# Kernel optimization log

Hardware: AMD Instinct MI355X
Metric: run time of the kernel (lower is better)

The kernel has to match this reference:

```python
import jax, jax.numpy as jnp
import numpy as np

D_MODEL = 1024
N_HEAD = 16
D_HEAD = D_MODEL // N_HEAD


def setup_inputs() -> dict:
    key = jax.random.key(0)
    ks = jax.random.split(key, 5)
    x = jax.random.normal(ks[0], (4, 2048, D_MODEL), dtype=jnp.float32)
    # qkv linear: weight [3*d_model, d_model], bias [3*d_model] (torch convention)
    w_qkv = jax.random.normal(ks[1], (3 * D_MODEL, D_MODEL), dtype=jnp.float32) / np.sqrt(D_MODEL)
    b_qkv = jnp.zeros((3 * D_MODEL,), dtype=jnp.float32)
    w_proj = jax.random.normal(ks[2], (D_MODEL, D_MODEL), dtype=jnp.float32) / np.sqrt(D_MODEL)
    b_proj = jnp.zeros((D_MODEL,), dtype=jnp.float32)
    return {"x": x, "w_qkv": w_qkv, "b_qkv": b_qkv, "w_proj": w_proj, "b_proj": b_proj}


def reference(x, w_qkv, b_qkv, w_proj, b_proj):
    B, T, C = x.shape
    qkv = x @ w_qkv.T + b_qkv  # [B,T,3C]
    q, k, v = jnp.split(qkv, 3, axis=-1)
    # [B, H, T, Dh]
    q = q.reshape(B, T, N_HEAD, D_HEAD).transpose(0, 2, 1, 3)
    k = k.reshape(B, T, N_HEAD, D_HEAD).transpose(0, 2, 1, 3)
    v = v.reshape(B, T, N_HEAD, D_HEAD).transpose(0, 2, 1, 3)
    att = jnp.einsum('bhqd,bhkd->bhqk', q, k) / jnp.sqrt(jnp.float32(D_HEAD))
    causal = jnp.tril(jnp.ones((T, T), dtype=bool))  # [T,T]
    att = jnp.where(causal, att, -jnp.inf)
    att = jax.nn.softmax(att, axis=-1)
    y = jnp.einsum('bhqk,bhkd->bhqd', att, v)  # [B,H,T,Dh]
    y = y.transpose(0, 2, 1, 3).reshape(B, T, C)
    return y @ w_proj.T + b_proj
```

## Files before the change

kernel.cpp:

```cpp
#include <hip/hip_runtime.h>
#include <hip/hip_bf16.h>

#define DEV static __device__ __forceinline__

typedef __attribute__((ext_vector_type(8))) short short8;
typedef __attribute__((ext_vector_type(4))) short short4v;
typedef __attribute__((ext_vector_type(4))) float float4v;
typedef __attribute__((ext_vector_type(4))) int int4v;

DEV unsigned short f2bf(float f) {
  unsigned int u = __builtin_bit_cast(unsigned int, f);
  u = (u + 0x7fffu + ((u >> 16) & 1u)) >> 16;
  return (unsigned short)u;
}

DEV __attribute__((address_space(3))) void* to_lds(void* p) {
  return (__attribute__((address_space(3))) void*)p;
}
DEV const __attribute__((address_space(1))) void* to_glb(const void* p) {
  return (const __attribute__((address_space(1))) void*)p;
}

DEV float4v zero4() { float4v z = {0.f, 0.f, 0.f, 0.f}; return z; }

DEV float ex2(float x) {
  float r;
  asm("v_exp_f32 %0, %1" : "=v"(r) : "v"(x));
  return r;
}
DEV unsigned int cvtpk(float lo, float hi) {
  unsigned int r;
  asm("v_cvt_pk_bf16_f32 %0, %1, %2" : "=v"(r) : "v"(lo), "v"(hi));
  return r;
}

__global__ __launch_bounds__(256)
void f32_to_bf16_kn(const float* __restrict__ src, unsigned short* __restrict__ dst, int n) {
  int i = (blockIdx.x * blockDim.x + threadIdx.x) * 4;
  int stride = gridDim.x * blockDim.x * 4;
  for (; i < n; i += stride) {
    float4v v = *reinterpret_cast<const float4v*>(src + i);
    short4v o;
    o[0] = (short)f2bf(v[0]);
    o[1] = (short)f2bf(v[1]);
    o[2] = (short)f2bf(v[2]);
    o[3] = (short)f2bf(v[3]);
    *reinterpret_cast<short4v*>(dst + i) = o;
  }
}

template<int EPI>
__global__ __launch_bounds__(256, 2)
void gemm_bt_kn(const unsigned short* __restrict__ A, const unsigned short* __restrict__ B,
                const float* __restrict__ bias, void* __restrict__ Cout,
                unsigned short* __restrict__ vtout, int M, int N, int K) {
  __shared__ unsigned short sA[128 * 64];
  __shared__ unsigned short sB[128 * 64];
  const int t = threadIdx.x;
  const int wave = t >> 6, lane = t & 63;
  const int wm = wave >> 1, wn = wave & 1;
  const int nwg = gridDim.x * gridDim.y;
  const int lid = blockIdx.y * gridDim.x + blockIdx.x;
  const int swz = (lid & 7) * (nwg >> 3) + (lid >> 3);
  const int m0 = (swz / gridDim.x) * 128, n0 = (swz % gridDim.x) * 128;
  const int l15 = lane & 15, l4 = lane >> 4;

  float4v acc[4][4];
#pragma unroll
  for (int i = 0; i < 4; i++)
#pragma unroll
    for (int j = 0; j < 4; j++) acc[i][j] = zero4();

  const int row_s = t >> 3;
  const int cols_s = ((t & 7) ^ ((t >> 3) & 7)) * 8;

  for (int k0 = 0; k0 < K; k0 += 64) {
    __syncthreads();
#pragma unroll
    for (int i = 0; i < 4; i++) {
      const unsigned short* ga = &A[(size_t)(m0 + row_s + i * 32) * K + k0 + cols_s];
      __builtin_amdgcn_global_load_lds(to_glb(ga), to_lds(&sA[(i * 4096 + wave * 1024) / 2]), 16, 0, 0);
    }
#pragma unroll
    for (int i = 0; i < 4; i++) {
      const unsigned short* gb = &B[(size_t)(n0 + row_s + i * 32) * K + k0 + cols_s];
      __builtin_amdgcn_global_load_lds(to_glb(gb), to_lds(&sB[(i * 4096 + wave * 1024) / 2]), 16, 0, 0);
    }
    __syncthreads();
#pragma unroll
    for (int kc = 0; kc < 2; kc++) {
      short8 af[4], bf[4];
#pragma unroll
      for (int mf = 0; mf < 4; mf++) {
        int off = ((wm * 64 + mf * 16 + l15) * 128 + kc * 64 + l4 * 16) ^ ((l15 & 7) << 4);
        af[mf] = *reinterpret_cast<const short8*>((const char*)sA + off);
      }
#pragma unroll
      for (int nf = 0; nf < 4; nf++) {
        int off = ((wn * 64 + nf * 16 + l15) * 128 + kc * 64 + l4 * 16) ^ ((l15 & 7) << 4);
        bf[nf] = *reinterpret_cast<const short8*>((const char*)sB + off);
      }
      __builtin_amdgcn_s_setprio(1);
#pragma unroll
      for (int mf = 0; mf < 4; mf++)
#pragma unroll
        for (int nf = 0; nf < 4; nf++)
          acc[mf][nf] = __builtin_amdgcn_mfma_f32_16x16x32_bf16(af[mf], bf[nf], acc[mf][nf], 0, 0, 0);
      __builtin_amdgcn_s_setprio(0);
    }
  }

#pragma unroll
  for (int mf = 0; mf < 4; mf++) {
    const int row0 = m0 + wm * 64 + mf * 16 + l4 * 4;
#pragma unroll
    for (int nf = 0; nf < 4; nf++) {
      const int col = n0 + wn * 64 + nf * 16 + l15;
      float vv[4];
#pragma unroll
      for (int r = 0; r < 4; r++) vv[r] = acc[mf][nf][r] + bias[col];
      if (EPI == 1) {
#pragma unroll
        for (int r = 0; r < 4; r++)
          ((float*)Cout)[(size_t)(row0 + r) * N + col] = vv[r];
      } else {
        if (col < 2048) {
          const float s = (col < 1024) ? 0.18033688f : 1.0f;
#pragma unroll
          for (int r = 0; r < 4; r++)
            ((unsigned short*)Cout)[(size_t)(row0 + r) * 2048 + col] = f2bf(vv[r] * s);
        } else {
          const int hv = col - 2048;
          const int R = ((row0 >> 11) * 16 + (hv >> 6)) * 64 + (hv & 63);
          const int tc = row0 & 2047;
          unsigned long long w = (unsigned long long)cvtpk(vv[0], vv[1]) |
                                 ((unsigned long long)cvtpk(vv[2], vv[3]) << 32);
          *(unsigned long long*)&vtout[(size_t)R * 2048 + tc] = w;
        }
      }
    }
  }
}

__global__ __launch_bounds__(256, 3)
void attn_kn(const unsigned short* __restrict__ qk, const unsigned short* __restrict__ vt,
             unsigned short* __restrict__ y) {
  __shared__ unsigned short sK[2][4096];
  __shared__ unsigned short sV[2][4096];
  __shared__ unsigned short sP[4][2048];
  const int t = threadIdx.x;
  const int wave = t >> 6, lane = t & 63;
  const int l15 = lane & 15, l4 = lane >> 4;
  const int bh = blockIdx.x, b = bh >> 4, h = bh & 15;
  const int yb_ = blockIdx.y;
  const int qt = ((yb_ >> 2) & 1) ? ((yb_ < 8) ? yb_ + 4 : yb_ - 12) : 15 - yb_;
  const int q0w = qt * 128 + wave * 32;
  const size_t base = (size_t)b * 2048 * 2048;
  const unsigned short* Qp = qk + base + h * 64;
  const unsigned short* Kp = Qp + 1024;
  const unsigned short* Vt = vt + (size_t)bh * 64 * 2048;
  unsigned short* yb = y + (size_t)b * 2048 * 1024 + h * 64;

  short8 ones8;
#pragma unroll
  for (int j = 0; j < 8; j++) ones8[j] = (short)0x3F80;

  short8 qf[2][2];
#pragma unroll
  for (int m = 0; m < 2; m++)
#pragma unroll
    for (int kc = 0; kc < 2; kc++)
      qf[m][kc] = *reinterpret_cast<const short8*>(
          &Qp[(size_t)(q0w + m * 16 + l15) * 2048 + kc * 32 + l4 * 8]);

  float4v o_acc[2][4];
#pragma unroll
  for (int m = 0; m < 2; m++)
#pragma unroll
    for (int f = 0; f < 4; f++) o_acc[m][f] = zero4();
  float4v acc_l[2] = {zero4(), zero4()};

  auto stage_k = [&](int kv0, int bi) {
#pragma unroll
    for (int i = 0; i < 2; i++) {
      int unit = t + i * 256;
      int row = unit >> 3, sl = unit & 7;
      const unsigned short* g = Kp + (size_t)(kv0 + row) * 2048 + (sl ^ (row & 7)) * 8;
      __builtin_amdgcn_global_load_lds(to_glb(g), to_lds(&sK[bi][unit * 8]), 16, 0, 0);
    }
  };
  auto stage_v = [&](int kv0, int bi) {
#pragma unroll
    for (int i = 0; i < 2; i++) {
      int unit = t + i * 256;
      int d = unit >> 3, sl = unit & 7;
      const unsigned short* g = Vt + (size_t)d * 2048 + kv0 + (sl ^ (d & 7)) * 8;
      __builtin_amdgcn_global_load_lds(to_glb(g), to_lds(&sV[bi][unit * 8]), 16, 0, 0);
    }
  };

  const int nt = 2 * qt + 2;
  stage_k(0, 0);
  stage_v(0, 0);
  __syncthreads();

  for (int ti = 0; ti < nt; ti++) {
    const int cur = ti & 1;
    const int kv0 = ti * 64;
    const bool last = (ti + 1 == nt);
    if (!last) { stage_k(kv0 + 64, cur ^ 1); stage_v(kv0 + 64, cur ^ 1); }

    if (kv0 <= q0w + 31) {
      const char* Kb = (const char*)sK[cur];
      const char* Vb = (const char*)sV[cur];
      char* Pb = (char*)sP[wave];

      float4v st[2][4];
#pragma unroll
      for (int m = 0; m < 2; m++)
#pragma unroll
        for (int c = 0; c < 4; c++) st[m][c] = zero4();
#pragma unroll
      for (int kc = 0; kc < 2; kc++) {
        short8 ka[4];
#pragma unroll
        for (int c = 0; c < 4; c++) {
          int off = ((c * 16 + l15) * 128 + kc * 64 + l4 * 16) ^ ((l15 & 7) << 4);
          ka[c] = *reinterpret_cast<const short8*>(Kb + off);
        }
        __builtin_amdgcn_s_setprio(1);
#pragma unroll
        for (int c = 0; c < 4; c++) {
          st[0][c] = __builtin_amdgcn_mfma_f32_16x16x32_bf16(ka[c], qf[0][kc], st[0][c], 0, 0, 0);
          st[1][c] = __builtin_amdgcn_mfma_f32_16x16x32_bf16(ka[c], qf[1][kc], st[1][c], 0, 0, 0);
        }
        __builtin_amdgcn_s_setprio(0);
      }

#pragma unroll
      for (int m = 0; m < 2; m++) {
        if (kv0 + 63 > q0w + m * 16) {
          const int qrow = q0w + m * 16 + l15;
#pragma unroll
          for (int c = 0; c < 4; c++)
#pragma unroll
            for (int r = 0; r < 4; r++) {
              int kv = kv0 + c * 16 + l4 * 4 + r;
              if (kv > qrow) st[m][c][r] = -1e30f;
            }
        }
#pragma unroll
        for (int c = 0; c < 4; c++) {
          float p0 = ex2(st[m][c][0]), p1 = ex2(st[m][c][1]);
          float p2 = ex2(st[m][c][2]), p3 = ex2(st[m][c][3]);
          unsigned long long w = (unsigned long long)cvtpk(p0, p1) |
                                 ((unsigned long long)cvtpk(p2, p3) << 32);
          int off = ((m * 16 + l15) * 128 + (c * 16 + l4 * 4) * 2) ^ ((l15 & 7) << 4);
          *(unsigned long long*)(Pb + off) = w;
        }
      }
      asm volatile("s_waitcnt lgkmcnt(0)" ::: "memory");
      __builtin_amdgcn_sched_barrier(0);

#pragma unroll
      for (int kc = 0; kc < 2; kc++) {
        short8 pa[2];
#pragma unroll
        for (int m = 0; m < 2; m++) {
          int off = ((m * 16 + l15) * 128 + kc * 64 + l4 * 16) ^ ((l15 & 7) << 4);
          pa[m] = *reinterpret_cast<const short8*>(Pb + off);
        }
        short8 vbf[4];
#pragma unroll
        for (int f = 0; f < 4; f++) {
          int d = f * 16 + l15;
          int off = (d * 128 + kc * 64 + l4 * 16) ^ ((d & 7) << 4);
          vbf[f] = *reinterpret_cast<const short8*>(Vb + off);
        }
        __builtin_amdgcn_s_setprio(1);
#pragma unroll
        for (int f = 0; f < 4; f++) {
          o_acc[0][f] = __builtin_amdgcn_mfma_f32_16x16x32_bf16(pa[0], vbf[f], o_acc[0][f], 0, 0, 0);
          o_acc[1][f] = __builtin_amdgcn_mfma_f32_16x16x32_bf16(pa[1], vbf[f], o_acc[1][f], 0, 0, 0);
        }
        acc_l[0] = __builtin_amdgcn_mfma_f32_16x16x32_bf16(pa[0], ones8, acc_l[0], 0, 0, 0);
        acc_l[1] = __builtin_amdgcn_mfma_f32_16x16x32_bf16(pa[1], ones8, acc_l[1], 0, 0, 0);
        __builtin_amdgcn_s_setprio(0);
      }
    }
    __syncthreads();
  }

#pragma unroll
  for (int m = 0; m < 2; m++) {
    float lr[4];
#pragma unroll
    for (int r = 0; r < 4; r++) lr[r] = 1.0f / acc_l[m][r];
#pragma unroll
    for (int f = 0; f < 4; f++)
#pragma unroll
      for (int r = 0; r < 4; r++) {
        int q = q0w + m * 16 + l4 * 4 + r;
        yb[(size_t)q * 1024 + f * 16 + l15] = f2bf(o_acc[m][f][r] * lr[r]);
      }
  }
}

extern "C" void kernel_launch(void* const* d_in, const int* in_sizes, int n_in,
                              void* d_out, int out_size, void* d_ws, size_t ws_size,
                              hipStream_t stream) {
  const float* x = (const float*)d_in[0];
  const float* w_qkv = (const float*)d_in[1];
  const float* b_qkv = (const float*)d_in[2];
  const float* w_proj = (const float*)d_in[3];
  const float* b_proj = (const float*)d_in[4];
  float* out = (float*)d_out;
  char* ws = (char*)d_ws;

  const int M = 4 * 2048;
  unsigned short* x_bf = (unsigned short*)ws;
  unsigned short* wqkv_bf = (unsigned short*)(ws + (22ull << 20));
  unsigned short* wproj_bf = (unsigned short*)(ws + (28ull << 20));
  unsigned short* qk_buf = (unsigned short*)(ws + (30ull << 20));
  unsigned short* vt = (unsigned short*)(ws + (62ull << 20));
  unsigned short* y_bf = x_bf;

  f32_to_bf16_kn<<<2048, 256, 0, stream>>>(x, x_bf, M * 1024);
  f32_to_bf16_kn<<<1024, 256, 0, stream>>>(w_qkv, wqkv_bf, 3072 * 1024);
  f32_to_bf16_kn<<<512, 256, 0, stream>>>(w_proj, wproj_bf, 1024 * 1024);

  gemm_bt_kn<2><<<dim3(3072 / 128, M / 128), 256, 0, stream>>>(
      x_bf, wqkv_bf, b_qkv, qk_buf, vt, M, 3072, 1024);

  attn_kn<<<dim3(64, 16), 256, 0, stream>>>(qk_buf, vt, y_bf);

  gemm_bt_kn<1><<<dim3(1024 / 128, M / 128), 256, 0, stream>>>(
      y_bf, wproj_bf, b_proj, out, nullptr, M, 1024, 1024);
}
```

Before: 157.0 us.

## Use 256-row double-buffered GEMM tiles with prefetch for QKV and projection

Result: no change. 157.7 us (+0.5%).

```diff
diff --git a/kernel.cpp b/kernel.cpp
--- a/kernel.cpp
+++ b/kernel.cpp
@@ -49,73 +49,110 @@
   }
 }
 
-template<int EPI>
-__global__ __launch_bounds__(256, 2)
-void gemm_bt_kn(const unsigned short* __restrict__ A, const unsigned short* __restrict__ B,
-                const float* __restrict__ bias, void* __restrict__ Cout,
-                unsigned short* __restrict__ vtout, int M, int N, int K) {
-  __shared__ unsigned short sA[128 * 64];
-  __shared__ unsigned short sB[128 * 64];
+template<int BN, int WM, int WN, int EPI>
+DEV void gemm256_body(const unsigned short* __restrict__ A, const unsigned short* __restrict__ B,
+                      const float* __restrict__ bias, void* __restrict__ Cout,
+                      unsigned short* __restrict__ vtout, int M, int N, int K,
+                      unsigned short* sAraw, unsigned short* sBraw) {
+  constexpr int MF = 256 / (WM * 16);
+  constexpr int NF = BN / (WN * 16);
+  constexpr int BPASS = BN / 64;
   const int t = threadIdx.x;
-  const int wave = t >> 6, lane = t & 63;
-  const int wm = wave >> 1, wn = wave & 1;
-  const int nwg = gridDim.x * gridDim.y;
-  const int lid = blockIdx.y * gridDim.x + blockIdx.x;
+  const int lane = t & 63;
+  const int wid = t >> 6;
+  const int l15 = lane & 15, l4 = lane >> 4;
+  const int wm = wid / WN, wn = wid % WN;
+  const int wrow = wm * MF * 16, wcol = wn * NF * 16;
+  const int gx = gridDim.x;
+  const int nwg = gx * gridDim.y;
+  const int lid = blockIdx.y * gx + blockIdx.x;
   const int swz = (lid & 7) * (nwg >> 3) + (lid >> 3);
-  const int m0 = (swz / gridDim.x) * 128, n0 = (swz % gridDim.x) * 128;
-  const int l15 = lane & 15, l4 = lane >> 4;
-
-  float4v acc[4][4];
-#pragma unroll
-  for (int i = 0; i < 4; i++)
-#pragma unroll
-    for (int j = 0; j < 4; j++) acc[i][j] = zero4();
-
-  const int row_s = t >> 3;
-  const int cols_s = ((t & 7) ^ ((t >> 3) & 7)) * 8;
-
-  for (int k0 = 0; k0 < K; k0 += 64) {
-    __syncthreads();
+  const int m0 = (swz / gx) * 256, n0 = (swz % gx) * BN;
+  const int lkey = (l15 & 7) << 4;
+
+  float4v acc[MF][NF];
+#pragma unroll
+  for (int i = 0; i < MF; i++)
+#pragma unroll
+    for (int j = 0; j < NF; j++) acc[i][j] = zero4();
+
+  auto stage = [&](int bi, int k0) {
 #pragma unroll
     for (int i = 0; i < 4; i++) {
-      const unsigned short* ga = &A[(size_t)(m0 + row_s + i * 32) * K + k0 + cols_s];
-      __builtin_amdgcn_global_load_lds(to_glb(ga), to_lds(&sA[(i * 4096 + wave * 1024) / 2]), 16, 0, 0);
-    }
-#pragma unroll
-    for (int i = 0; i < 4; i++) {
-      const unsigned short* gb = &B[(size_t)(n0 + row_s + i * 32) * K + k0 + cols_s];
-      __builtin_amdgcn_global_load_lds(to_glb(gb), to_lds(&sB[(i * 4096 + wave * 1024) / 2]), 16, 0, 0);
-    }
-    __syncthreads();
-#pragma unroll
-    for (int kc = 0; kc < 2; kc++) {
-      short8 af[4], bf[4];
-#pragma unroll
-      for (int mf = 0; mf < 4; mf++) {
-        int off = ((wm * 64 + mf * 16 + l15) * 128 + kc * 64 + l4 * 16) ^ ((l15 & 7) << 4);
-        af[mf] = *reinterpret_cast<const short8*>((const char*)sA + off);
-      }
-#pragma unroll
-      for (int nf = 0; nf < 4; nf++) {
-        int off = ((wn * 64 + nf * 16 + l15) * 128 + kc * 64 + l4 * 16) ^ ((l15 & 7) << 4);
-        bf[nf] = *reinterpret_cast<const short8*>((const char*)sB + off);
-      }
+      int unit = t + i * 512;
+      int row = unit >> 3, sl = unit & 7;
+      const unsigned short* g = &A[(size_t)(m0 + row) * K + k0 + (sl ^ (row & 7)) * 8];
+      __builtin_amdgcn_global_load_lds(to_glb(g), to_lds(&sAraw[bi * 256 * 64 + unit * 8]), 16, 0, 0);
+    }
+#pragma unroll
+    for (int i = 0; i < BPASS; i++) {
+      int unit = t + i * 512;
+      int row = unit >> 3, sl = unit & 7;
+      const unsigned short* g = &B[(size_t)(n0 + row) * K + k0 + (sl ^ (row & 7)) * 8];
+      __builtin_amdgcn_global_load_lds(to_glb(g), to_lds(&sBraw[bi * BN * 64 + unit * 8]), 16, 0, 0);
+    }
+  };
+
+  stage(0, 0);
+  const int nk = K >> 6;
+  for (int s = 0; s < nk; ++s) {
+    const int cur = s & 1;
+    if (s + 1 < nk) {
+      stage(cur ^ 1, (s + 1) << 6);
+      if constexpr (BPASS == 3)
+        asm volatile("s_waitcnt vmcnt(7)");
+      else
+        asm volatile("s_waitcnt vmcnt(6)");
+    } else {
+      asm volatile("s_waitcnt vmcnt(0)");
+    }
+    __builtin_amdgcn_sched_barrier(0);
+    __builtin_amdgcn_s_barrier();
+    __builtin_amdgcn_sched_barrier(0);
+
+    const char* Ab = (const char*)&sAraw[cur * 256 * 64];
+    const char* Bb = (const char*)&sBraw[cur * BN * 64];
+    short8 bfr[NF][2];
+#pragma unroll
+    for (int nf = 0; nf < NF; nf++)
+#pragma unroll
+      for (int kc = 0; kc < 2; kc++) {
+        int off = ((wcol + nf * 16 + l15) * 128 + kc * 64 + l4 * 16) ^ lkey;
+        bfr[nf][kc] = *reinterpret_cast<const short8*>(Bb + off);
+      }
+#pragma unroll
+    for (int g = 0; g < MF; g += 4) {
+      short8 afr[4][2];
+#pragma unroll
+      for (int i = 0; i < 4; i++)
+#pragma unroll
+        for (int kc = 0; kc < 2; kc++) {
+          int off = ((wrow + (g + i) * 16 + l15) * 128 + kc * 64 + l4 * 16) ^ lkey;
+          afr[i][kc] = *reinterpret_cast<const short8*>(Ab + off);
+        }
       __builtin_amdgcn_s_setprio(1);
 #pragma unroll
-      for (int mf = 0; mf < 4; mf++)
-#pragma unroll
-        for (int nf = 0; nf < 4; nf++)
-          acc[mf][nf] = __builtin_amdgcn_mfma_f32_16x16x32_bf16(af[mf], bf[nf], acc[mf][nf], 0, 0, 0);
+      for (int kc = 0; kc < 2; kc++)
+#pragma unroll
+        for (int i = 0; i < 4; i++)
+#pragma unroll
+          for (int nf = 0; nf < NF; nf++)
+            acc[g + i][nf] =
+                __builtin_amdgcn_mfma_f32_16x16x32_bf16(afr[i][kc], bfr[nf][kc], acc[g + i][nf], 0, 0, 0);
       __builtin_amdgcn_s_setprio(0);
     }
-  }
-
-#pragma unroll
-  for (int mf = 0; mf < 4; mf++) {
-    const int row0 = m0 + wm * 64 + mf * 16 + l4 * 4;
-#pragma unroll
-    for (int nf = 0; nf < 4; nf++) {
-      const int col = n0 + wn * 64 + nf * 16 + l15;
+    asm volatile("s_waitcnt lgkmcnt(0)" ::: "memory");
+    __builtin_amdgcn_sched_barrier(0);
+    __builtin_amdgcn_s_barrier();
+    __builtin_amdgcn_sched_barrier(0);
+  }
+
+#pragma unroll
+  for (int mf = 0; mf < MF; mf++) {
+    const int row0 = m0 + wrow + mf * 16 + l4 * 4;
+#pragma unroll
+    for (int nf = 0; nf < NF; nf++) {
+      const int col = n0 + wcol + nf * 16 + l15;
       float vv[4];
 #pragma unroll
       for (int r = 0; r < 4; r++) vv[r] = acc[mf][nf][r] + bias[col];
@@ -125,10 +162,10 @@
           ((float*)Cout)[(size_t)(row0 + r) * N + col] = vv[r];
       } else {
         if (col < 2048) {
-          const float s = (col < 1024) ? 0.18033688f : 1.0f;
+          const float sc = (col < 1024) ? 0.18033688f : 1.0f;
 #pragma unroll
           for (int r = 0; r < 4; r++)
-            ((unsigned short*)Cout)[(size_t)(row0 + r) * 2048 + col] = f2bf(vv[r] * s);
+            ((unsigned short*)Cout)[(size_t)(row0 + r) * 2048 + col] = f2bf(vv[r] * sc);
         } else {
           const int hv = col - 2048;
           const int R = ((row0 >> 11) * 16 + (hv >> 6)) * 64 + (hv & 63);
@@ -140,6 +177,24 @@
       }
     }
   }
+}
+
+__global__ __launch_bounds__(512, 2)
+void gemm256_qkv_kn(const unsigned short* __restrict__ A, const unsigned short* __restrict__ B,
+                    const float* __restrict__ bias, unsigned short* __restrict__ qkout,
+                    unsigned short* __restrict__ vtout, int M, int N, int K) {
+  __shared__ unsigned short sA[2][256 * 64];
+  __shared__ unsigned short sB[2][192 * 64];
+  gemm256_body<192, 2, 4, 2>(A, B, bias, qkout, vtout, M, N, K, &sA[0][0], &sB[0][0]);
+}
+
+__global__ __launch_bounds__(512, 2)
+void gemm256_proj_kn(const unsigned short* __restrict__ A, const unsigned short* __restrict__ B,
+                     const float* __restrict__ bias, float* __restrict__ Cout,
+                     int M, int N, int K) {
+  __shared__ unsigned short sA[2][256 * 64];
+  __shared__ unsigned short sB[2][128 * 64];
+  gemm256_body<128, 4, 2, 1>(A, B, bias, Cout, nullptr, M, N, K, &sA[0][0], &sB[0][0]);
 }
 
 __global__ __launch_bounds__(256, 3)
@@ -329,11 +384,11 @@
   f32_to_bf16_kn<<<1024, 256, 0, stream>>>(w_qkv, wqkv_bf, 3072 * 1024);
   f32_to_bf16_kn<<<512, 256, 0, stream>>>(w_proj, wproj_bf, 1024 * 1024);
 
-  gemm_bt_kn<2><<<dim3(3072 / 128, M / 128), 256, 0, stream>>>(
+  gemm256_qkv_kn<<<dim3(16, 32), 512, 0, stream>>>(
       x_bf, wqkv_bf, b_qkv, qk_buf, vt, M, 3072, 1024);
 
   attn_kn<<<dim3(64, 16), 256, 0, stream>>>(qk_buf, vt, y_bf);
 
-  gemm_bt_kn<1><<<dim3(1024 / 128, M / 128), 256, 0, stream>>>(
-      y_bf, wproj_bf, b_proj, out, nullptr, M, 1024, 1024);
-}
+  gemm256_proj_kn<<<dim3(8, 32), 512, 0, stream>>>(
+      y_bf, wproj_bf, b_proj, out, M, 1024, 1024);
+}
```

## Replace GEMMs with 8-wave double-buffered 256-row tile kernels with interleaved loads

Applied to the files above, without the earlier changes.

Result: no change. 160.0 us (+1.9%).

```diff
diff --git a/kernel.cpp b/kernel.cpp
--- a/kernel.cpp
+++ b/kernel.cpp
@@ -49,73 +49,145 @@
   }
 }
 
-template<int EPI>
-__global__ __launch_bounds__(256, 2)
-void gemm_bt_kn(const unsigned short* __restrict__ A, const unsigned short* __restrict__ B,
-                const float* __restrict__ bias, void* __restrict__ Cout,
-                unsigned short* __restrict__ vtout, int M, int N, int K) {
-  __shared__ unsigned short sA[128 * 64];
-  __shared__ unsigned short sB[128 * 64];
-  const int t = threadIdx.x;
-  const int wave = t >> 6, lane = t & 63;
-  const int wm = wave >> 1, wn = wave & 1;
-  const int nwg = gridDim.x * gridDim.y;
-  const int lid = blockIdx.y * gridDim.x + blockIdx.x;
+template<int NF, int EPI>
+DEV void gemm8p_body(const unsigned short* __restrict__ A, const unsigned short* __restrict__ B,
+                     const float* __restrict__ bias, void* __restrict__ Cout,
+                     unsigned short* __restrict__ vtout, int M, int N, int K,
+                     unsigned short* sA, unsigned short* sB) {
+  constexpr int BN = NF * 64;
+  const int t = threadIdx.x, lane = t & 63, wid = t >> 6;
+  const int l15 = lane & 15, l4 = lane >> 4;
+  const int wm = wid >> 2, wn = wid & 3;
+  const int wrow = wm * 128, wcol = wn * NF * 16;
+  const int gx = gridDim.x, nwg = gx * gridDim.y;
+  const int lid = blockIdx.y * gx + blockIdx.x;
   const int swz = (lid & 7) * (nwg >> 3) + (lid >> 3);
-  const int m0 = (swz / gridDim.x) * 128, n0 = (swz % gridDim.x) * 128;
-  const int l15 = lane & 15, l4 = lane >> 4;
-
-  float4v acc[4][4];
-#pragma unroll
-  for (int i = 0; i < 4; i++)
-#pragma unroll
-    for (int j = 0; j < 4; j++) acc[i][j] = zero4();
-
-  const int row_s = t >> 3;
-  const int cols_s = ((t & 7) ^ ((t >> 3) & 7)) * 8;
-
-  for (int k0 = 0; k0 < K; k0 += 64) {
-    __syncthreads();
-#pragma unroll
-    for (int i = 0; i < 4; i++) {
-      const unsigned short* ga = &A[(size_t)(m0 + row_s + i * 32) * K + k0 + cols_s];
-      __builtin_amdgcn_global_load_lds(to_glb(ga), to_lds(&sA[(i * 4096 + wave * 1024) / 2]), 16, 0, 0);
+  const int m0 = (swz / gx) * 256, n0 = (swz % gx) * BN;
+  const int lkey = (l15 & 7) << 4;
+
+  float4v acc[8][NF];
+#pragma unroll
+  for (int i = 0; i < 8; i++)
+#pragma unroll
+    for (int j = 0; j < NF; j++) acc[i][j] = zero4();
+
+  auto stB = [&](int buf, int k0, int pass) {
+    int u = t + pass * 512, row = u >> 3, sl = u & 7;
+    const unsigned short* g = &B[(size_t)(n0 + row) * K + k0 + (sl ^ (row & 7)) * 8];
+    __builtin_amdgcn_global_load_lds(to_glb(g), to_lds(&sB[buf * BN * 64 + u * 8]), 16, 0, 0);
+  };
+  auto stA = [&](int buf, int k0, int q) {
+    int r6 = t >> 3, sl = t & 7;
+    int row = 32 * q + (r6 & 31) + 128 * (r6 >> 5);
+    const unsigned short* g = &A[(size_t)(m0 + row) * K + k0 + (sl ^ (row & 7)) * 8];
+    __builtin_amdgcn_global_load_lds(to_glb(g), to_lds(&sA[buf * 256 * 64 + row * 64 + sl * 8]), 16, 0, 0);
+  };
+  short8 af[2][2], bfr[NF][2];
+  auto rdA = [&](const char* Ab, int q) {
+#pragma unroll
+    for (int fi = 0; fi < 2; fi++)
+#pragma unroll
+      for (int kc = 0; kc < 2; kc++) {
+        int off = ((wrow + (q * 2 + fi) * 16 + l15) * 128 + kc * 64 + l4 * 16) ^ lkey;
+        af[fi][kc] = *reinterpret_cast<const short8*>(Ab + off);
+      }
+  };
+  auto rdB = [&](const char* Bb) {
+#pragma unroll
+    for (int nf = 0; nf < NF; nf++)
+#pragma unroll
+      for (int kc = 0; kc < 2; kc++) {
+        int off = ((wcol + nf * 16 + l15) * 128 + kc * 64 + l4 * 16) ^ lkey;
+        bfr[nf][kc] = *reinterpret_cast<const short8*>(Bb + off);
+      }
+  };
+
+#define MMQ(Q)                                                                           \
+  do {                                                                                   \
+    __builtin_amdgcn_s_setprio(1);                                                       \
+    _Pragma("unroll") for (int kc = 0; kc < 2; kc++)                                     \
+        _Pragma("unroll") for (int fi = 0; fi < 2; fi++)                                 \
+            _Pragma("unroll") for (int nf = 0; nf < NF; nf++) acc[(Q)*2 + fi][nf] =      \
+        __builtin_amdgcn_mfma_f32_16x16x32_bf16(af[fi][kc], bfr[nf][kc],                 \
+                                                acc[(Q)*2 + fi][nf], 0, 0, 0);           \
+    __builtin_amdgcn_s_setprio(0);                                                       \
+  } while (0)
+#define BARR __builtin_amdgcn_s_barrier()
+#define LGKM0 asm volatile("s_waitcnt lgkmcnt(0)" ::: "memory")
+#define VMW(N) asm volatile("s_waitcnt vmcnt(" #N ")" ::: "memory")
+
+#pragma unroll
+  for (int p = 0; p < NF; p++) stB(0, 0, p);
+#pragma unroll
+  for (int q = 0; q < 4; q++) stA(0, 0, q);
+  VMW(3);
+  BARR;
+
+  const char* Ab0 = (const char*)&sA[0];
+  const char* Bb0 = (const char*)&sB[0];
+  const char* Ab1 = (const char*)&sA[256 * 64];
+  const char* Bb1 = (const char*)&sB[BN * 64];
+  const int NI = K >> 7;
+
+  for (int i = 0; i < NI; ++i) {
+    const int k1 = (i << 7) + 64, k2 = (i << 7) + 128;
+    const bool nl = (i + 1 < NI);
+    rdB(Bb0);
+    rdA(Ab0, 0);
+    stB(1, k1, 0);
+    stB(1, k1, 1);
+    VMW(4);
+    BARR; LGKM0; MMQ(0); BARR;
+    rdA(Ab0, 1);
+    if (NF == 3) { stB(1, k1, 2); stA(1, k1, 0); }
+    else { stA(1, k1, 0); stA(1, k1, 1); }
+    VMW(5);
+    BARR; LGKM0; MMQ(1); BARR;
+    rdA(Ab0, 2);
+    if (NF == 3) { stA(1, k1, 1); stA(1, k1, 2); }
+    else { stA(1, k1, 2); stA(1, k1, 3); }
+    VMW(6);
+    BARR; LGKM0; MMQ(2); BARR;
+    rdA(Ab0, 3);
+    if (NF == 3) stA(1, k1, 3);
+    VMW(3);
+    BARR; LGKM0; MMQ(3); BARR;
+    rdB(Bb1);
+    rdA(Ab1, 0);
+    if (nl) { stB(0, k2, 0); stB(0, k2, 1); VMW(4); } else { VMW(2); }
+    BARR; LGKM0; MMQ(0); BARR;
+    rdA(Ab1, 1);
+    if (nl) {
+      if (NF == 3) { stB(0, k2, 2); stA(0, k2, 0); }
+      else { stA(0, k2, 0); stA(0, k2, 1); }
+      VMW(5);
+    } else { VMW(1); }
+    BARR; LGKM0; MMQ(1); BARR;
+    rdA(Ab1, 2);
+    if (nl) {
+      if (NF == 3) { stA(0, k2, 1); stA(0, k2, 2); }
+      else { stA(0, k2, 2); stA(0, k2, 3); }
+      VMW(6);
+    } else { VMW(0); }
+    BARR; LGKM0; MMQ(2); BARR;
+    rdA(Ab1, 3);
+    if (nl) {
+      if (NF == 3) stA(0, k2, 3);
+      VMW(3);
     }
-#pragma unroll
-    for (int i = 0; i < 4; i++) {
-      const unsigned short* gb = &B[(size_t)(n0 + row_s + i * 32) * K + k0 + cols_s];
-      __builtin_amdgcn_global_load_lds(to_glb(gb), to_lds(&sB[(i * 4096 + wave * 1024) / 2]), 16, 0, 0);
-    }
-    __syncthreads();
-#pragma unroll
-    for (int kc = 0; kc < 2; kc++) {
-      short8 af[4], bf[4];
-#pragma unroll
-      for (int mf = 0; mf < 4; mf++) {
-        int off = ((wm * 64 + mf * 16 + l15) * 128 + kc * 64 + l4 * 16) ^ ((l15 & 7) << 4);
-        af[mf] = *reinterpret_cast<const short8*>((const char*)sA + off);
-      }
-#pragma unroll
-      for (int nf = 0; nf < 4; nf++) {
-        int off = ((wn * 64 + nf * 16 + l15) * 128 + kc * 64 + l4 * 16) ^ ((l15 & 7) << 4);
-        bf[nf] = *reinterpret_cast<const short8*>((const char*)sB + off);
-      }
-      __builtin_amdgcn_s_setprio(1);
-#pragma unroll
-      for (int mf = 0; mf < 4; mf++)
-#pragma unroll
-        for (int nf = 0; nf < 4; nf++)
-          acc[mf][nf] = __builtin_amdgcn_mfma_f32_16x16x32_bf16(af[mf], bf[nf], acc[mf][nf], 0, 0, 0);
-      __builtin_amdgcn_s_setprio(0);
-    }
+    BARR; LGKM0; MMQ(3); BARR;
   }
-
-#pragma unroll
-  for (int mf = 0; mf < 4; mf++) {
-    const int row0 = m0 + wm * 64 + mf * 16 + l4 * 4;
-#pragma unroll
-    for (int nf = 0; nf < 4; nf++) {
-      const int col = n0 + wn * 64 + nf * 16 + l15;
+#undef MMQ
+#undef BARR
+#undef LGKM0
+#undef VMW
+
+#pragma unroll
+  for (int mf = 0; mf < 8; mf++) {
+    const int row0 = m0 + wrow + mf * 16 + l4 * 4;
+#pragma unroll
+    for (int nf = 0; nf < NF; nf++) {
+      const int col = n0 + wcol + nf * 16 + l15;
       float vv[4];
 #pragma unroll
       for (int r = 0; r < 4; r++) vv[r] = acc[mf][nf][r] + bias[col];
@@ -125,10 +197,10 @@
           ((float*)Cout)[(size_t)(row0 + r) * N + col] = vv[r];
       } else {
         if (col < 2048) {
-          const float s = (col < 1024) ? 0.18033688f : 1.0f;
+          const float sc = (col < 1024) ? 0.18033688f : 1.0f;
 #pragma unroll
           for (int r = 0; r < 4; r++)
-            ((unsigned short*)Cout)[(size_t)(row0 + r) * 2048 + col] = f2bf(vv[r] * s);
+            ((unsigned short*)Cout)[(size_t)(row0 + r) * 2048 + col] = f2bf(vv[r] * sc);
         } else {
           const int hv = col - 2048;
           const int R = ((row0 >> 11) * 16 + (hv >> 6)) * 64 + (hv & 63);
@@ -140,6 +212,24 @@
       }
     }
   }
+}
+
+__global__ __launch_bounds__(512, 2)
+void gemm8p_qkv_kn(const unsigned short* __restrict__ A, const unsigned short* __restrict__ B,
+                   const float* __restrict__ bias, unsigned short* __restrict__ qkout,
+                   unsigned short* __restrict__ vtout, int M, int N, int K) {
+  __shared__ unsigned short sA[2 * 256 * 64];
+  __shared__ unsigned short sB[2 * 192 * 64];
+  gemm8p_body<3, 2>(A, B, bias, qkout, vtout, M, N, K, sA, sB);
+}
+
+__global__ __launch_bounds__(512, 2)
+void gemm8p_proj_kn(const unsigned short* __restrict__ A, const unsigned short* __restrict__ B,
+                    const float* __restrict__ bias, float* __restrict__ Cout,
+                    int M, int N, int K) {
+  __shared__ unsigned short sA[2 * 256 * 64];
+  __shared__ unsigned short sB[2 * 128 * 64];
+  gemm8p_body<2, 1>(A, B, bias, Cout, nullptr, M, N, K, sA, sB);
 }
 
 __global__ __launch_bounds__(256, 3)
@@ -329,11 +419,11 @@
   f32_to_bf16_kn<<<1024, 256, 0, stream>>>(w_qkv, wqkv_bf, 3072 * 1024);
   f32_to_bf16_kn<<<512, 256, 0, stream>>>(w_proj, wproj_bf, 1024 * 1024);
 
-  gemm_bt_kn<2><<<dim3(3072 / 128, M / 128), 256, 0, stream>>>(
+  gemm8p_qkv_kn<<<dim3(16, 32), 512, 0, stream>>>(
       x_bf, wqkv_bf, b_qkv, qk_buf, vt, M, 3072, 1024);
 
   attn_kn<<<dim3(64, 16), 256, 0, stream>>>(qk_buf, vt, y_bf);
 
-  gemm_bt_kn<1><<<dim3(1024 / 128, M / 128), 256, 0, stream>>>(
-      y_bf, wproj_bf, b_proj, out, nullptr, M, 1024, 1024);
-}
+  gemm8p_proj_kn<<<dim3(8, 32), 512, 0, stream>>>(
+      y_bf, wproj_bf, b_proj, out, M, 1024, 1024);
+}
```
